# Optimization experiments

Measured on AMD Instinct MI355X. Metric: run time of the kernel, lower is better.

The kernel has to match this reference:

```python
import jax, jax.numpy as jnp
import numpy as np

N_NODES = 200000
N_EDGES = 1250000
N_RELS = 8
IN_F, HID_F, OUT_F = 64, 64, 32


def setup_inputs() -> dict:
    key = jax.random.key(0)
    ks = jax.random.split(key, 8)
    x = jax.random.normal(ks[0], (N_NODES, IN_F), dtype=jnp.float32)
    edge_index = jax.random.randint(ks[1], (2, N_EDGES), 0, N_NODES, dtype=jnp.int64)
    edge_type = jax.random.randint(ks[2], (N_EDGES,), 0, N_RELS, dtype=jnp.int64)
    # Glorot-ish scaled params
    weight1 = jax.random.normal(ks[3], (N_RELS, IN_F, HID_F), dtype=jnp.float32) / np.sqrt(IN_F)
    root1 = jax.random.normal(ks[4], (IN_F, HID_F), dtype=jnp.float32) / np.sqrt(IN_F)
    bias1 = jnp.zeros((HID_F,), dtype=jnp.float32)
    weight2 = jax.random.normal(ks[5], (N_RELS, HID_F, OUT_F), dtype=jnp.float32) / np.sqrt(HID_F)
    root2 = jax.random.normal(ks[6], (HID_F, OUT_F), dtype=jnp.float32) / np.sqrt(HID_F)
    bias2 = jnp.zeros((OUT_F,), dtype=jnp.float32)
    return {"x": x, "edge_index": edge_index, "edge_type": edge_type,
            "weight1": weight1, "root1": root1, "bias1": bias1,
            "weight2": weight2, "root2": root2, "bias2": bias2}


def _rgcn_conv(x, edge_src, edge_dst, edge_type, weight, root, bias):
    """PyG RGCNConv: per-relation mean aggregation + root transform + bias."""
    num_nodes = x.shape[0]
    num_rels = weight.shape[0]
    # Transform every node under every relation weight: [N, R, H]
    xw = jnp.einsum('nd,rdh->nrh', x, weight)
    # Per-edge message: source node transformed by the edge's relation weight
    msgs = xw[edge_src, edge_type]  # [E, H]
    # Per-(target node, relation) mean aggregation
    seg = edge_dst * num_rels + edge_type  # combined segment id
    num_seg = num_nodes * num_rels
    sums = jax.ops.segment_sum(msgs, seg, num_segments=num_seg)  # [N*R, H]
    cnts = jax.ops.segment_sum(jnp.ones((msgs.shape[0],), dtype=x.dtype), seg,
                               num_segments=num_seg)
    mean = sums / jnp.maximum(cnts, 1.0)[:, None]
    agg = mean.reshape(num_nodes, num_rels, -1).sum(axis=1)  # sum over relations
    return agg + x @ root + bias


def reference(x, edge_index, edge_type, weight1, root1, bias1, weight2, root2, bias2):
    edge_src, edge_dst = edge_index[0], edge_index[1]
    h = _rgcn_conv(x, edge_src, edge_dst, edge_type, weight1, root1, bias1)
    h = jax.nn.relu(h)
    out = _rgcn_conv(h, edge_src, edge_dst, edge_type, weight2, root2, bias2)
    return out
```

## Files before the change

kernel.cpp:

```cpp
#include <hip/hip_runtime.h>

#define N_NODES 200000
#define N_EDGES 1250000
#define N_RELS 8
#define NROWS 1600000
#define NROWS_PAD 1601536
#define NSCAN 782
#define NBUCK 6250

#define NB_COUNT 4883
#define NB_XCAST 6250
#define NB_PREP1 144
#define NB_PREP2 72

typedef __attribute__((ext_vector_type(8))) short short8v;
typedef __attribute__((ext_vector_type(4))) float f32x4;

__device__ __forceinline__ ushort rne_bf16(float v) {
  unsigned u = __float_as_uint(v);
  return (ushort)((u + 0x7FFFu + ((u >> 16) & 1u)) >> 16);
}


__device__ __forceinline__ void prep_body(const float* W, const float* Root,
                                          ushort* Bf, int ncol, int i) {
  int col = i / 576, k = i - col * 576;
  float w = (k < 512) ? W[k * ncol + col] : Root[(k - 512) * ncol + col];
  int WN = ncol >> 4;
  int ks = k >> 5, kg = (k >> 3) & 3, j = k & 7;
  int wn = col >> 4, l15 = col & 15;
  int lane = (kg << 4) | l15;
  Bf[(ks * WN + wn) * 512 + lane * 8 + j] = rne_bf16(w);
}

__global__ __launch_bounds__(256) void k_setup(
    const int* __restrict__ ei, const int* __restrict__ et, int* __restrict__ cnt,
    int* __restrict__ er,
    const float* __restrict__ x, ushort* __restrict__ xbf,
    const float* __restrict__ w1, const float* __restrict__ r1, ushort* __restrict__ bf1,
    const float* __restrict__ w2, const float* __restrict__ r2, ushort* __restrict__ bf2) {
  int blk = blockIdx.x, t = threadIdx.x;
  if (blk < NB_COUNT) {
    int e = blk * 256 + t;
    if (e < N_EDGES) {
      int dst = ei[N_EDGES + e];
      int r = et[e];
      er[e] = atomicAdd(&cnt[dst * N_RELS + r], 1);
    }
  } else if (blk < NB_COUNT + NB_XCAST) {
    int i = (blk - NB_COUNT) * 256 + t;
    float4 a = ((const float4*)x)[i * 2];
    float4 b = ((const float4*)x)[i * 2 + 1];
    union { uint4 q; ushort u[8]; } o;
    o.u[0] = rne_bf16(a.x); o.u[1] = rne_bf16(a.y);
    o.u[2] = rne_bf16(a.z); o.u[3] = rne_bf16(a.w);
    o.u[4] = rne_bf16(b.x); o.u[5] = rne_bf16(b.y);
    o.u[6] = rne_bf16(b.z); o.u[7] = rne_bf16(b.w);
    ((uint4*)xbf)[i] = o.q;
  } else if (blk < NB_COUNT + NB_XCAST + NB_PREP1) {
    int i = (blk - NB_COUNT - NB_XCAST) * 256 + t;
    prep_body(w1, r1, bf1, 64, i);
  } else {
    int i = (blk - NB_COUNT - NB_XCAST - NB_PREP1) * 256 + t;
    prep_body(w2, r2, bf2, 32, i);
  }
}


__global__ __launch_bounds__(256) void k_bsum(const int* __restrict__ cnt,
                                              int* __restrict__ bsum) {
  __shared__ int sh[256];
  int b = blockIdx.x, t = threadIdx.x;
  const int4* p = (const int4*)(cnt + b * 2048);
  int4 v0 = p[2 * t], v1 = p[2 * t + 1];
  int s = v0.x + v0.y + v0.z + v0.w + v1.x + v1.y + v1.z + v1.w;
  sh[t] = s;
  __syncthreads();
  for (int o = 128; o >= 1; o >>= 1) {
    if (t < o) sh[t] += sh[t + o];
    __syncthreads();
  }
  if (t == 0) bsum[b] = sh[0];
}

__global__ __launch_bounds__(1024) void k_scan1(const int* __restrict__ bsum,
                                                int* __restrict__ bpre,
                                                int* __restrict__ rowoff) {
  __shared__ int sh[1024];
  int t = threadIdx.x;
  int v = (t < NSCAN) ? bsum[t] : 0;
  sh[t] = v;
  __syncthreads();
  for (int o = 1; o < 1024; o <<= 1) {
    int a = (t >= o) ? sh[t - o] : 0;
    __syncthreads();
    sh[t] += a;
    __syncthreads();
  }
  if (t < NSCAN) bpre[t] = sh[t] - v;
  if (t == 0) rowoff[NROWS] = N_EDGES;
}

__global__ __launch_bounds__(256) void k_apply(const int* __restrict__ cnt,
                                               const int* __restrict__ bpre,
                                               int* __restrict__ rowoff) {
  __shared__ int sh[256];
  int b = blockIdx.x, t = threadIdx.x;
  const int4* p = (const int4*)(cnt + b * 2048);
  int4 v0 = p[2 * t], v1 = p[2 * t + 1];
  int v[8] = {v0.x, v0.y, v0.z, v0.w, v1.x, v1.y, v1.z, v1.w};
  int s = 0;
#pragma unroll
  for (int j = 0; j < 8; ++j) s += v[j];
  sh[t] = s;
  __syncthreads();
  for (int o = 1; o < 256; o <<= 1) {
    int a = (t >= o) ? sh[t - o] : 0;
    __syncthreads();
    sh[t] += a;
    __syncthreads();
  }
  int run = bpre[b] + sh[t] - s;
  int base = b * 2048 + t * 8;
#pragma unroll
  for (int j = 0; j < 8; ++j) {
    int i = base + j;
    if (i < NROWS) rowoff[i] = run;
    run += v[j];
  }
}

__global__ void k_scatter(const int* __restrict__ ei, const int* __restrict__ et,
                          const int* __restrict__ rowoff, const int* __restrict__ er,
                          int* __restrict__ ep) {
  int e = blockIdx.x * 256 + threadIdx.x;
  if (e < N_EDGES) {
    int src = ei[e];
    int dst = ei[N_EDGES + e];
    int r = et[e];
    int row = dst * N_RELS + r;
    int pos = rowoff[row] + er[e];
    ep[pos] = src | ((row & 255) << 18);
  }
}


template <int NCOL, bool RELUOUT, bool OUTBF>
__global__ __launch_bounds__(512, 8) void k_rgcn(
    const ushort* __restrict__ Xg, const ushort* __restrict__ Bf,
    const float* __restrict__ Bias, const int* __restrict__ rowoff,
    const int* __restrict__ ep, void* __restrict__ OutP) {
  __shared__ __align__(16) ushort agg[256 * 64];
  __shared__ int loff[260];
  __shared__ int wsplit[12];
  __shared__ __align__(16) float bias_lds[64];

  int t = threadIdx.x;
  int b = blockIdx.x;
  int d0 = b * 32;
  int lane = t & 63, w = t >> 6;

  {
    uint4 zz = make_uint4(0, 0, 0, 0);
    uint4* a4 = (uint4*)agg;
#pragma unroll
    for (int q = 0; q < 4; ++q) a4[t + q * 512] = zz;
  }
  if (t < 257) loff[t] = rowoff[b * 256 + t];
  if (t < NCOL) bias_lds[t] = Bias[t];
  __syncthreads();
  if (t < 9) {
    int s0 = loff[0], ntot = loff[256] - s0;
    int target = s0 + ((ntot * t) >> 3);
    int lo = 0, hi = 256;
    while (lo < hi) {
      int mid = (lo + hi) >> 1;
      if (loff[mid] < target) lo = mid + 1; else hi = mid;
    }
    wsplit[t] = lo;
  }
  __syncthreads();

  {
    int s = __builtin_amdgcn_readfirstlane(loff[wsplit[w]]);
    int e = __builtin_amdgcn_readfirstlane(loff[wsplit[w + 1]]);
    int n = e - s;
    const int* wep = ep + s;
    const char* Xb = (const char*)Xg;
    unsigned lane2 = (unsigned)(lane << 1);
    int cur = -1, nrun = 0;
    float a = 0.f;

#define FLUSH()                                                         \
    {                                                                   \
      float m = a * __builtin_amdgcn_rcpf((float)nrun);                 \
      int sw = (cur << 6) + (lane ^ (((cur >> 3) & 7) << 3));           \
      agg[sw] = rne_bf16(m);                                            \
    }

    int i = 0;
    for (; i + 8 <= n; i += 8) {
      int pk[8];
#pragma unroll
      for (int u = 0; u < 8; ++u)
        pk[u] = __builtin_amdgcn_readfirstlane(wep[i + u]);
      ushort hv[8];
#pragma unroll
      for (int u = 0; u < 8; ++u)
        hv[u] = *(const ushort*)(Xb + ((((unsigned)pk[u] & 0x3FFFFu) << 7) + lane2));
#pragma unroll
      for (int u = 0; u < 8; ++u) {
        int row = (int)((unsigned)pk[u] >> 18);
        float v = __uint_as_float((unsigned)hv[u] << 16);
        if (row != cur) {
          if (cur >= 0) FLUSH();
          cur = row; a = 0.f; nrun = 0;
        }
        a += v; ++nrun;
      }
    }
    for (; i < n; ++i) {
      int pk = __builtin_amdgcn_readfirstlane(wep[i]);
      ushort hv = *(const ushort*)(Xb + ((((unsigned)pk & 0x3FFFFu) << 7) + lane2));
      int row = (int)((unsigned)pk >> 18);
      float v = __uint_as_float((unsigned)hv << 16);
      if (row != cur) {
        if (cur >= 0) FLUSH();
        cur = row; a = 0.f; nrun = 0;
      }
      a += v; ++nrun;
    }
    if (cur >= 0) FLUSH();
#undef FLUSH
  }
  __syncthreads();

  int l15 = lane & 15, kg = lane >> 4;
  f32x4 acc = {0.f, 0.f, 0.f, 0.f};

  if constexpr (NCOL == 64) {
    int wm = w >> 2, wn = w & 3;
    int col = wn * 16 + l15;
    for (int ks = 0; ks < 18; ++ks) {
      union { uint4 q; short8v s; } bh, ah;
      bh.q = *(const uint4*)(Bf + (ks * 4 + wn) * 512 + lane * 8);
      if (ks < 16) {
        int rr = ks >> 1;
        int f0 = ((ks & 1) << 5) + (kg << 3);
        int row = ((wm * 16 + l15) << 3) + rr;
        int sw = (row << 6) + (f0 ^ ((l15 & 7) << 3));
        ah.q = *(const uint4*)&agg[sw];
      } else {
        int kb = ((ks - 16) << 5) + (kg << 3);
        ah.q = *(const uint4*)&Xg[(size_t)(d0 + wm * 16 + l15) * 64 + kb];
      }
      acc = __builtin_amdgcn_mfma_f32_16x16x32_bf16(ah.s, bh.s, acc, 0, 0, 0);
    }
    __syncthreads();
#pragma unroll
    for (int i2 = 0; i2 < 4; ++i2) {
      float v = acc[i2] + bias_lds[col];
      if (RELUOUT) v = fmaxf(v, 0.f);
      agg[(wm * 16 + kg * 4 + i2) * 64 + col] = rne_bf16(v);
    }
    __syncthreads();
    {
      int r = t >> 4, c4 = t & 15;
      uint2 v = *(const uint2*)&agg[r * 64 + c4 * 4];
      if (OUTBF) {
        ((uint2*)OutP)[(size_t)(d0 + r) * 16 + c4] = v;
      } else {
        ((uint2*)OutP)[(size_t)(d0 + r) * 16 + c4] = v;
      }
    }
  } else {
    int wm = w >> 2, wn = (w >> 1) & 1, ksp = w & 1;
    int col = wn * 16 + l15;
    for (int ks = ksp; ks < 18; ks += 2) {
      union { uint4 q; short8v s; } bh, ah;
      bh.q = *(const uint4*)(Bf + (ks * 2 + wn) * 512 + lane * 8);
      if (ks < 16) {
        int rr = ks >> 1;
        int f0 = ((ks & 1) << 5) + (kg << 3);
        int row = ((wm * 16 + l15) << 3) + rr;
        int sw = (row << 6) + (f0 ^ ((l15 & 7) << 3));
        ah.q = *(const uint4*)&agg[sw];
      } else {
        int kb = ((ks - 16) << 5) + (kg << 3);
        ah.q = *(const uint4*)&Xg[(size_t)(d0 + wm * 16 + l15) * 64 + kb];
      }
      acc = __builtin_amdgcn_mfma_f32_16x16x32_bf16(ah.s, bh.s, acc, 0, 0, 0);
    }
    __syncthreads();
    float* red = (float*)agg;
    int rbase = wm * 16 + kg * 4;
    if (ksp == 1) {
#pragma unroll
      for (int i2 = 0; i2 < 4; ++i2) red[(rbase + i2) * 36 + col] = acc[i2];
    }
    __syncthreads();
    if (ksp == 0) {
#pragma unroll
      for (int i2 = 0; i2 < 4; ++i2) {
        float v = acc[i2] + red[(rbase + i2) * 36 + col] + bias_lds[col];
        if (RELUOUT) v = fmaxf(v, 0.f);
        ((float*)OutP)[(size_t)(d0 + rbase + i2) * 32 + col] = v;
      }
    }
  }
}


extern "C" void kernel_launch(void* const* d_in, const int* in_sizes, int n_in,
                              void* d_out, int out_size, void* d_ws, size_t ws_size,
                              hipStream_t stream) {
  const float* x = (const float*)d_in[0];
  const int* ei = (const int*)d_in[1];
  const int* et = (const int*)d_in[2];
  const float* w1 = (const float*)d_in[3];
  const float* r1 = (const float*)d_in[4];
  const float* b1 = (const float*)d_in[5];
  const float* w2 = (const float*)d_in[6];
  const float* r2 = (const float*)d_in[7];
  const float* b2 = (const float*)d_in[8];
  float* out = (float*)d_out;

  int* cnt = (int*)d_ws;
  int* bsum = cnt + NROWS_PAD;
  int* bpre = bsum + 1024;
  int* rowoff = bpre + 1024;
  int* er = rowoff + NROWS + 16;
  int* ep = er + N_EDGES;
  ushort* bf1 = (ushort*)(ep + N_EDGES);
  ushort* bf2 = bf1 + 36864;
  ushort* xbf = bf2 + 18432;
  ushort* hbf = xbf + 12800000;

  hipMemsetAsync(cnt, 0, (size_t)NROWS_PAD * 4, stream);
  k_setup<<<NB_COUNT + NB_XCAST + NB_PREP1 + NB_PREP2, 256, 0, stream>>>(
      ei, et, cnt, er, x, xbf, w1, r1, bf1, w2, r2, bf2);
  k_bsum<<<NSCAN, 256, 0, stream>>>(cnt, bsum);
  k_scan1<<<1, 1024, 0, stream>>>(bsum, bpre, rowoff);
  k_apply<<<NSCAN, 256, 0, stream>>>(cnt, bpre, rowoff);
  k_scatter<<<(N_EDGES + 255) / 256, 256, 0, stream>>>(ei, et, rowoff, er, ep);

  k_rgcn<64, true, true><<<NBUCK, 512, 0, stream>>>(xbf, bf1, b1, rowoff, ep, hbf);
  k_rgcn<32, false, false><<<NBUCK, 512, 0, stream>>>(hbf, bf2, b2, rowoff, ep, out);
}
```

Measured before the change: 276.3 us.

## Split each wave into four 16-lane edge groups with 8-byte gathers

The gather-aggregate phase now splits each block's edge range into 32 segments, one per 16-lane quarter-wave, instead of one per wave. Each lane gathers four bf16 features with one 8-byte load instead of one 2-byte load, and the edge payloads are loaded cooperatively and broadcast by shuffle, with the next batch prefetched. The aim is fewer, wider memory transactions and more independent work per wave. In exchange, groups within a wave wait for the longest segment, register pressure rises (launch bounds lowered from 8 to 6), and bf16 rounding changes from round-to-nearest-even to round-half-up.

```diff
diff --git a/kernel.cpp b/kernel.cpp
--- a/kernel.cpp
+++ b/kernel.cpp
@@ -146,13 +146,13 @@
 
 
 template <int NCOL, bool RELUOUT, bool OUTBF>
-__global__ __launch_bounds__(512, 8) void k_rgcn(
+__global__ __launch_bounds__(512, 6) void k_rgcn(
     const ushort* __restrict__ Xg, const ushort* __restrict__ Bf,
     const float* __restrict__ Bias, const int* __restrict__ rowoff,
     const int* __restrict__ ep, void* __restrict__ OutP) {
   __shared__ __align__(16) ushort agg[256 * 64];
   __shared__ int loff[260];
-  __shared__ int wsplit[12];
+  __shared__ int wsplit[36];
   __shared__ __align__(16) float bias_lds[64];
 
   int t = threadIdx.x;
@@ -169,9 +169,9 @@
   if (t < 257) loff[t] = rowoff[b * 256 + t];
   if (t < NCOL) bias_lds[t] = Bias[t];
   __syncthreads();
-  if (t < 9) {
+  if (t < 33) {
     int s0 = loff[0], ntot = loff[256] - s0;
-    int target = s0 + ((ntot * t) >> 3);
+    int target = s0 + (int)(((long long)ntot * t) >> 5);
     int lo = 0, hi = 256;
     while (lo < hi) {
       int mid = (lo + hi) >> 1;
@@ -182,56 +182,78 @@
   __syncthreads();
 
   {
-    int s = __builtin_amdgcn_readfirstlane(loff[wsplit[w]]);
-    int e = __builtin_amdgcn_readfirstlane(loff[wsplit[w + 1]]);
-    int n = e - s;
-    const int* wep = ep + s;
+    int g = lane >> 4;
+    int q = lane & 15;
+    int rlo = wsplit[(w << 2) + g];
+    int rhi = wsplit[(w << 2) + g + 1];
+    int gs = loff[rlo];
+    int ge = loff[rhi];
+    int n = ge - gs;
+    int nm = n;
+    { int s2 = __shfl_xor(nm, 16); nm = nm > s2 ? nm : s2;
+      s2 = __shfl_xor(nm, 32); nm = nm > s2 ? nm : s2; }
+    int nmax = nm;
+
     const char* Xb = (const char*)Xg;
-    unsigned lane2 = (unsigned)(lane << 1);
-    int cur = -1, nrun = 0;
-    float a = 0.f;
-
-#define FLUSH()                                                         \
-    {                                                                   \
-      float m = a * __builtin_amdgcn_rcpf((float)nrun);                 \
-      int sw = (cur << 6) + (lane ^ (((cur >> 3) & 7) << 3));           \
-      agg[sw] = rne_bf16(m);                                            \
-    }
-
-    int i = 0;
-    for (; i + 8 <= n; i += 8) {
-      int pk[8];
-#pragma unroll
-      for (int u = 0; u < 8; ++u)
-        pk[u] = __builtin_amdgcn_readfirstlane(wep[i + u]);
-      ushort hv[8];
-#pragma unroll
-      for (int u = 0; u < 8; ++u)
-        hv[u] = *(const ushort*)(Xb + ((((unsigned)pk[u] & 0x3FFFFu) << 7) + lane2));
-#pragma unroll
-      for (int u = 0; u < 8; ++u) {
+    unsigned qoff = (unsigned)(q << 3);
+    float a0 = 0.f, a1 = 0.f, a2 = 0.f, a3 = 0.f, nrunf = 0.f;
+    int cur = -1;
+
+#define FLUSH4()                                                              \
+    {                                                                         \
+      float r_ = __builtin_amdgcn_rcpf(nrunf);                                \
+      float m0 = a0 * r_, m1 = a1 * r_, m2 = a2 * r_, m3 = a3 * r_;           \
+      unsigned p0 = ((__float_as_uint(m1) + 0x8000u) & 0xFFFF0000u) |         \
+                    ((__float_as_uint(m0) + 0x8000u) >> 16);                  \
+      unsigned p1 = ((__float_as_uint(m3) + 0x8000u) & 0xFFFF0000u) |         \
+                    ((__float_as_uint(m2) + 0x8000u) >> 16);                  \
+      int us = (cur << 6) + ((((q >> 1) ^ ((cur >> 3) & 7)) << 3) |           \
+                             ((q & 1) << 2));                                 \
+      *(uint2*)&agg[us] = make_uint2(p0, p1);                                 \
+    }
+
+    int pi = gs + q;
+    if (pi > ge - 1) pi = ge - 1;
+    if (pi < 0) pi = 0;
+    int pay = ep[pi];
+
+    for (int base = 0; base < nmax; base += 16) {
+      int pk[16]; uint2 hv[16];
+#pragma unroll
+      for (int u = 0; u < 16; ++u) {
+        pk[u] = __shfl(pay, (g << 4) | u);
+        hv[u] = *(const uint2*)(Xb + ((((unsigned)pk[u] & 0x3FFFFu) << 7) + qoff));
+      }
+      {
+        int nb2 = base + 16;
+        if (nb2 < nmax) {
+          int p2 = gs + nb2 + q;
+          if (p2 > ge - 1) p2 = ge - 1;
+          if (p2 < 0) p2 = 0;
+          pay = ep[p2];
+        }
+      }
+#pragma unroll
+      for (int u = 0; u < 16; ++u) {
+        bool active = (base + u) < n;
         int row = (int)((unsigned)pk[u] >> 18);
-        float v = __uint_as_float((unsigned)hv[u] << 16);
-        if (row != cur) {
-          if (cur >= 0) FLUSH();
-          cur = row; a = 0.f; nrun = 0;
+        unsigned x0 = hv[u].x, x1 = hv[u].y;
+        float v0 = __uint_as_float(x0 << 16);
+        float v1 = __uint_as_float(x0 & 0xFFFF0000u);
+        float v2 = __uint_as_float(x1 << 16);
+        float v3 = __uint_as_float(x1 & 0xFFFF0000u);
+        if (active) {
+          if (row != cur) {
+            if (cur >= 0) FLUSH4();
+            cur = row; a0 = v0; a1 = v1; a2 = v2; a3 = v3; nrunf = 1.f;
+          } else {
+            a0 += v0; a1 += v1; a2 += v2; a3 += v3; nrunf += 1.f;
+          }
         }
-        a += v; ++nrun;
-      }
-    }
-    for (; i < n; ++i) {
-      int pk = __builtin_amdgcn_readfirstlane(wep[i]);
-      ushort hv = *(const ushort*)(Xb + ((((unsigned)pk & 0x3FFFFu) << 7) + lane2));
-      int row = (int)((unsigned)pk >> 18);
-      float v = __uint_as_float((unsigned)hv << 16);
-      if (row != cur) {
-        if (cur >= 0) FLUSH();
-        cur = row; a = 0.f; nrun = 0;
-      }
-      a += v; ++nrun;
-    }
-    if (cur >= 0) FLUSH();
-#undef FLUSH
+      }
+    }
+    if (cur >= 0) FLUSH4();
+#undef FLUSH4
   }
   __syncthreads();
 
@@ -267,11 +289,7 @@
     {
       int r = t >> 4, c4 = t & 15;
       uint2 v = *(const uint2*)&agg[r * 64 + c4 * 4];
-      if (OUTBF) {
-        ((uint2*)OutP)[(size_t)(d0 + r) * 16 + c4] = v;
-      } else {
-        ((uint2*)OutP)[(size_t)(d0 + r) * 16 + c4] = v;
-      }
+      ((uint2*)OutP)[(size_t)(d0 + r) * 16 + c4] = v;
     }
   } else {
     int wm = w >> 2, wn = (w >> 1) & 1, ksp = w & 1;
```

Result: no change. 279.0 us (+1.0%).

## Stage gathered neighbor rows into LDS via async global_load_lds double buffering

Applied to the files above, without the earlier changes.

Replaces the per-lane 2-byte gathers of source-node features with 16-byte global_load_lds transfers. Each wave fetches 8 neighbor rows per slot into a double-buffered LDS stage and waits with explicit vmcnt, so the next group's loads overlap the current group's accumulation. It also switches the flush rounding to a cheaper round-half-up bf16 conversion, which changes rounding slightly. The cost is 16 KB of extra LDS per block, which may lower occupancy under the 512x8 launch bounds.

```diff
diff --git a/kernel.cpp b/kernel.cpp
--- a/kernel.cpp
+++ b/kernel.cpp
@@ -151,6 +151,7 @@
     const float* __restrict__ Bias, const int* __restrict__ rowoff,
     const int* __restrict__ ep, void* __restrict__ OutP) {
   __shared__ __align__(16) ushort agg[256 * 64];
+  __shared__ __align__(16) ushort stage[8 * 1024];
   __shared__ int loff[260];
   __shared__ int wsplit[12];
   __shared__ __align__(16) float bias_lds[64];
@@ -186,8 +187,7 @@
     int e = __builtin_amdgcn_readfirstlane(loff[wsplit[w + 1]]);
     int n = e - s;
     const int* wep = ep + s;
-    const char* Xb = (const char*)Xg;
-    unsigned lane2 = (unsigned)(lane << 1);
+    ushort* stage_w = stage + (w << 10);
     int cur = -1, nrun = 0;
     float a = 0.f;
 
@@ -195,42 +195,82 @@
     {                                                                   \
       float m = a * __builtin_amdgcn_rcpf((float)nrun);                 \
       int sw = (cur << 6) + (lane ^ (((cur >> 3) & 7) << 3));           \
-      agg[sw] = rne_bf16(m);                                            \
-    }
-
-    int i = 0;
-    for (; i + 8 <= n; i += 8) {
-      int pk[8];
-#pragma unroll
-      for (int u = 0; u < 8; ++u)
-        pk[u] = __builtin_amdgcn_readfirstlane(wep[i + u]);
-      ushort hv[8];
-#pragma unroll
-      for (int u = 0; u < 8; ++u)
-        hv[u] = *(const ushort*)(Xb + ((((unsigned)pk[u] & 0x3FFFFu) << 7) + lane2));
-#pragma unroll
-      for (int u = 0; u < 8; ++u) {
-        int row = (int)((unsigned)pk[u] >> 18);
-        float v = __uint_as_float((unsigned)hv[u] << 16);
-        if (row != cur) {
-          if (cur >= 0) FLUSH();
-          cur = row; a = 0.f; nrun = 0;
+      agg[sw] = (ushort)((__float_as_uint(m) + 0x8000u) >> 16);         \
+    }
+#define ISSUE(G)                                                              \
+    {                                                                         \
+      int i0_ = (G) << 3;                                                     \
+      int cmx_ = n - 1;                                                       \
+      int j_;                                                                 \
+      j_ = i0_ + 0; if (j_ > cmx_) j_ = cmx_;                                 \
+      int p0_ = __builtin_amdgcn_readfirstlane(wep[j_]);                      \
+      j_ = i0_ + 1; if (j_ > cmx_) j_ = cmx_;                                 \
+      int p1_ = __builtin_amdgcn_readfirstlane(wep[j_]);                      \
+      j_ = i0_ + 2; if (j_ > cmx_) j_ = cmx_;                                 \
+      int p2_ = __builtin_amdgcn_readfirstlane(wep[j_]);                      \
+      j_ = i0_ + 3; if (j_ > cmx_) j_ = cmx_;                                 \
+      int p3_ = __builtin_amdgcn_readfirstlane(wep[j_]);                      \
+      j_ = i0_ + 4; if (j_ > cmx_) j_ = cmx_;                                 \
+      int p4_ = __builtin_amdgcn_readfirstlane(wep[j_]);                      \
+      j_ = i0_ + 5; if (j_ > cmx_) j_ = cmx_;                                 \
+      int p5_ = __builtin_amdgcn_readfirstlane(wep[j_]);                      \
+      j_ = i0_ + 6; if (j_ > cmx_) j_ = cmx_;                                 \
+      int p6_ = __builtin_amdgcn_readfirstlane(wep[j_]);                      \
+      j_ = i0_ + 7; if (j_ > cmx_) j_ = cmx_;                                 \
+      int p7_ = __builtin_amdgcn_readfirstlane(wep[j_]);                      \
+      int jj_ = lane >> 3;                                                    \
+      int t0_ = (jj_ & 1) ? p1_ : p0_;                                        \
+      int t1_ = (jj_ & 1) ? p3_ : p2_;                                        \
+      int t2_ = (jj_ & 1) ? p5_ : p4_;                                        \
+      int t3_ = (jj_ & 1) ? p7_ : p6_;                                        \
+      int u0_ = (jj_ & 2) ? t1_ : t0_;                                        \
+      int u1_ = (jj_ & 2) ? t3_ : t2_;                                        \
+      int se_ = (jj_ & 4) ? u1_ : u0_;                                        \
+      const ushort* gp_ =                                                     \
+          Xg + (((unsigned)se_ & 0x3FFFFu) << 6) + ((lane & 7) << 3);         \
+      __builtin_amdgcn_global_load_lds(                                       \
+          (const __attribute__((address_space(1))) void*)gp_,                 \
+          (__attribute__((address_space(3))) void*)(stage_w + (((G) & 1) << 9)), \
+          16, 0, 0);                                                          \
+    }
+#define CONSUME(G, NV)                                                        \
+    {                                                                         \
+      int i0_ = (G) << 3;                                                     \
+      const ushort* sb_ = stage_w + (((G) & 1) << 9);                         \
+      _Pragma("unroll")                                                       \
+      for (int u_ = 0; u_ < 8; ++u_) {                                        \
+        if (u_ < (NV)) {                                                      \
+          int pk_ = __builtin_amdgcn_readfirstlane(wep[i0_ + u_]);            \
+          ushort hv_ = sb_[(u_ << 6) + lane];                                 \
+          int row_ = (int)((unsigned)pk_ >> 18);                              \
+          float v_ = __uint_as_float((unsigned)hv_ << 16);                    \
+          if (row_ != cur) {                                                  \
+            if (cur >= 0) FLUSH();                                            \
+            cur = row_; a = 0.f; nrun = 0;                                    \
+          }                                                                   \
+          a += v_; ++nrun;                                                    \
+        }                                                                     \
+      }                                                                       \
+    }
+
+    if (n > 0) {
+      int nslots = (n + 7) >> 3;
+      ISSUE(0);
+      if (nslots > 1) ISSUE(1);
+      for (int g = 0; g < nslots; ++g) {
+        if (g + 1 < nslots) {
+          asm volatile("s_waitcnt vmcnt(1)" ::: "memory");
+        } else {
+          asm volatile("s_waitcnt vmcnt(0)" ::: "memory");
         }
-        a += v; ++nrun;
+        int nv = n - (g << 3); if (nv > 8) nv = 8;
+        CONSUME(g, nv);
+        if (g + 2 < nslots) ISSUE(g + 2);
       }
-    }
-    for (; i < n; ++i) {
-      int pk = __builtin_amdgcn_readfirstlane(wep[i]);
-      ushort hv = *(const ushort*)(Xb + ((((unsigned)pk & 0x3FFFFu) << 7) + lane2));
-      int row = (int)((unsigned)pk >> 18);
-      float v = __uint_as_float((unsigned)hv << 16);
-      if (row != cur) {
-        if (cur >= 0) FLUSH();
-        cur = row; a = 0.f; nrun = 0;
-      }
-      a += v; ++nrun;
-    }
-    if (cur >= 0) FLUSH();
+      if (cur >= 0) FLUSH();
+    }
+#undef CONSUME
+#undef ISSUE
 #undef FLUSH
   }
   __syncthreads();
@@ -267,11 +307,7 @@
     {
       int r = t >> 4, c4 = t & 15;
       uint2 v = *(const uint2*)&agg[r * 64 + c4 * 4];
-      if (OUTBF) {
-        ((uint2*)OutP)[(size_t)(d0 + r) * 16 + c4] = v;
-      } else {
-        ((uint2*)OutP)[(size_t)(d0 + r) * 16 + c4] = v;
-      }
+      ((uint2*)OutP)[(size_t)(d0 + r) * 16 + c4] = v;
     }
   } else {
     int wm = w >> 2, wn = (w >> 1) & 1, ksp = w & 1;
```

After: 300.4 us. 8.7% more time.
